# Performance work log

Hardware: AMD Instinct MI355X
Metric: run time of the kernel (lower is better)

Reference implementation:

```python
import jax, jax.numpy as jnp
import numpy as np

N = 50000   # nodes
E = 800000  # edges
D = 128     # in_dim == hidden_dim
L = 3       # 1 + hidden_layers(=2) SAGEConv layers
G = 64      # graphs in batch
C = 10      # classes


def setup_inputs() -> dict:
    key = jax.random.key(0)
    ks = jax.random.split(key, 10)
    h = jax.random.normal(ks[0], (N, D), dtype=jnp.float32)
    src = jax.random.randint(ks[1], (E,), 0, N, dtype=jnp.int32)
    dst = jax.random.randint(ks[2], (E,), 0, N, dtype=jnp.int32)
    graph_id = jnp.sort(jax.random.randint(ks[3], (N,), 0, G, dtype=jnp.int32))
    scale = 1.0 / np.sqrt(D)
    w_self = jax.random.normal(ks[4], (L, D, D), dtype=jnp.float32) * scale
    w_neigh = jax.random.normal(ks[5], (L, D, D), dtype=jnp.float32) * scale
    b = jax.random.normal(ks[6], (L, D), dtype=jnp.float32) * 0.01
    w_cls = jax.random.normal(ks[7], (D, C), dtype=jnp.float32) * scale
    b_cls = jax.random.normal(ks[8], (C,), dtype=jnp.float32) * 0.01
    return {"h": h, "src": src, "dst": dst, "graph_id": graph_id,
            "num_graphs": G, "w_self": w_self, "w_neigh": w_neigh,
            "b": b, "w_cls": w_cls, "b_cls": b_cls}


def reference(h, src, dst, graph_id, num_graphs, w_self, w_neigh, b, w_cls, b_cls):
    n = h.shape[0]
    # in-degree for mean aggregation (nodes with no in-edges -> 0 neigh feat)
    deg = jax.ops.segment_sum(jnp.ones((src.shape[0],), h.dtype), dst,
                              num_segments=n)
    inv_deg = (1.0 / jnp.maximum(deg, 1.0))[:, None]  # [N,1]
    for l in range(L):
        msg = h[src]                                           # gather [E,D]
        agg = jax.ops.segment_sum(msg, dst, num_segments=n) * inv_deg  # mean
        h = jax.nn.relu(h @ w_self[l] + agg @ w_neigh[l] + b[l])
    # mean_nodes readout over batched graphs
    counts = jax.ops.segment_sum(jnp.ones((n,), h.dtype), graph_id,
                                 num_segments=num_graphs)
    hg = jax.ops.segment_sum(h, graph_id, num_segments=num_graphs)
    hg = hg / jnp.maximum(counts, 1.0)[:, None]                # [G,D]
    return hg @ w_cls + b_cls                                  # [G,C]
```

## Files before the change

kernel.cpp:

```cpp
#include <hip/hip_runtime.h>

typedef short bf16x8 __attribute__((ext_vector_type(8)));
typedef float f32x4 __attribute__((ext_vector_type(4)));

#define DIM 128
#define NLAYER 3
#define NG 64
#define NC 10
#define NXCD 8
#define MAXDEG 64
#define LROWE 136

static __device__ __forceinline__ float b2f(unsigned short u) {
  union { unsigned int i; float f; } x; x.i = ((unsigned int)u) << 16; return x.f;
}
static __device__ __forceinline__ unsigned short f2b(float f) {
  unsigned int x = __float_as_uint(f);
  unsigned int r = (x + 0x7FFFu + ((x >> 16) & 1u)) >> 16;
  return (unsigned short)r;
}


__global__ __launch_bounds__(256) void k_prep(const float* __restrict__ h0,
    const float* __restrict__ wself, const float* __restrict__ wneigh,
    unsigned short* __restrict__ h_a, unsigned short* __restrict__ wtS,
    unsigned short* __restrict__ wtN, int* __restrict__ cur,
    float* __restrict__ hg, int n) {
  int tid = blockIdx.x * 256 + threadIdx.x;
  int nthr = gridDim.x * 256;
  for (int i = tid; i < n; i += nthr) cur[i] = 0;
  for (int i = tid; i < NG * DIM; i += nthr) hg[i] = 0.f;
  int tot4 = n * (DIM / 4);
  for (int i = tid; i < tot4; i += nthr) {
    float4 v = *(const float4*)(h0 + (size_t)i * 4);
    ushort4 r;
    r.x = f2b(v.x); r.y = f2b(v.y); r.z = f2b(v.z); r.w = f2b(v.w);
    *(ushort4*)(h_a + (size_t)i * 4) = r;
  }
  int totw = NLAYER * DIM * DIM;
  for (int i = tid; i < totw; i += nthr) {
    int l = i >> 14, rem = i & 16383, c = rem >> 7, k = rem & 127;
    int sidx = (l << 14) + (k << 7) + c;
    wtS[i] = f2b(wself[sidx]);
    wtN[i] = f2b(wneigh[sidx]);
  }
}


__global__ __launch_bounds__(256) void k_fillp(const int* __restrict__ src,
    const int* __restrict__ dst, int* __restrict__ cur, int* __restrict__ colxp,
    int e, int n) {
  int bucket = blockIdx.x & (NXCD - 1);
  int chunk = blockIdx.x >> 3, nchunk = gridDim.x >> 3;
  int bs = (n + NXCD - 1) / NXCD;
  int lo = bucket * bs, hi = min(n, lo + bs);
  for (int i = chunk * 256 + threadIdx.x; i < e; i += nchunk * 256) {
    int d = __builtin_nontemporal_load(dst + i);
    if (d >= lo && d < hi) {
      int p = atomicAdd(&cur[d], 1);
      if (p < MAXDEG) colxp[(size_t)d * MAXDEG + p] = __builtin_nontemporal_load(src + i);
    }
  }
}


__global__ __launch_bounds__(256, 4) void k_agg(const unsigned short* __restrict__ h,
    const int* __restrict__ cur, const int* __restrict__ colxp,
    unsigned short* __restrict__ agg, int n) {
  int wv = threadIdx.x >> 6, lane = threadIdx.x & 63;
  int v = blockIdx.x * 4 + wv;
  if (v >= n) return;
  int deg = cur[v];
  int end = min(deg, MAXDEG);
  const int4* cp4 = (const int4*)(colxp + (size_t)v * MAXDEG);
  int off = lane * 2;
  float a0[4], a1[4];
  #pragma unroll
  for (int k = 0; k < 4; ++k) { a0[k] = 0.f; a1[k] = 0.f; }
  for (int i = 0; i < end; i += 16) {
    int4 c0 = cp4[(i >> 2) + 0];
    int4 c1 = cp4[(i >> 2) + 1];
    int4 c2 = cp4[(i >> 2) + 2];
    int4 c3 = cp4[(i >> 2) + 3];
    int idxv[16] = {c0.x, c0.y, c0.z, c0.w, c1.x, c1.y, c1.z, c1.w,
                    c2.x, c2.y, c2.z, c2.w, c3.x, c3.y, c3.z, c3.w};
    unsigned int pk[16];
    #pragma unroll
    for (int k = 0; k < 16; ++k) {
      int s = (i + k < end) ? idxv[k] : 0;
      unsigned int p = *(const unsigned int*)(h + (size_t)s * DIM + off);
      pk[k] = (i + k < end) ? p : 0u;
    }
    #pragma unroll
    for (int k = 0; k < 16; ++k) {
      a0[k & 3] += __uint_as_float(pk[k] << 16);
      a1[k & 3] += __uint_as_float(pk[k] & 0xFFFF0000u);
    }
  }
  float s0 = (a0[0] + a0[1]) + (a0[2] + a0[3]);
  float s1 = (a1[0] + a1[1]) + (a1[2] + a1[3]);
  float w = 1.0f / fmaxf((float)deg, 1.0f);
  unsigned int outpk = (unsigned int)f2b(s0 * w) | ((unsigned int)f2b(s1 * w) << 16);
  *(unsigned int*)(agg + (size_t)v * DIM + off) = outpk;
}


__global__ __launch_bounds__(512, 2) void k_gemm(const unsigned short* __restrict__ hin,
    const unsigned short* __restrict__ agg, const unsigned short* __restrict__ wtS,
    const unsigned short* __restrict__ wtN, const float* __restrict__ bias,
    unsigned short* __restrict__ hout, int n) {
  __shared__ unsigned short ldsA[16 * LROWE];
  __shared__ unsigned short ldsG[16 * LROWE];
  int lane = threadIdx.x & 63, wv = threadIdx.x >> 6;
  int r = lane & 15, q = lane >> 4;
  int cf = wv;
  const unsigned short* wsp = wtS + (size_t)(cf * 16 + r) * DIM + q * 8;
  const unsigned short* wnp = wtN + (size_t)(cf * 16 + r) * DIM + q * 8;
  bf16x8 ws[4], wn[4];
  #pragma unroll
  for (int kf = 0; kf < 4; ++kf) {
    ws[kf] = *(const bf16x8*)(wsp + kf * 32);
    wn[kf] = *(const bf16x8*)(wnp + kf * 32);
  }
  int col = cf * 16 + r;
  float bval = bias[col];
  int ntiles = (n + 15) >> 4;
  int st = threadIdx.x & 255;
  int srow = st >> 4, schunk = st & 15;
  bool doG = threadIdx.x >= 256;
  for (int tb = blockIdx.x; tb < ntiles; tb += gridDim.x) {
    int row0 = tb * 16;
    {
      int grow = row0 + srow; if (grow > n - 1) grow = n - 1;
      const unsigned short* sp = (doG ? agg : hin) + (size_t)grow * DIM + schunk * 8;
      unsigned short* dp = (doG ? ldsG : ldsA) + srow * LROWE + schunk * 8;
      *(int4*)dp = *(const int4*)sp;
    }
    __syncthreads();
    bf16x8 ah[4], ag[4];
    #pragma unroll
    for (int kf = 0; kf < 4; ++kf) {
      ah[kf] = *(const bf16x8*)(ldsA + r * LROWE + q * 8 + kf * 32);
      ag[kf] = *(const bf16x8*)(ldsG + r * LROWE + q * 8 + kf * 32);
    }
    f32x4 acc = {0.f, 0.f, 0.f, 0.f};
    #pragma unroll
    for (int kf = 0; kf < 4; ++kf)
      acc = __builtin_amdgcn_mfma_f32_16x16x32_bf16(ah[kf], ws[kf], acc, 0, 0, 0);
    #pragma unroll
    for (int kf = 0; kf < 4; ++kf)
      acc = __builtin_amdgcn_mfma_f32_16x16x32_bf16(ag[kf], wn[kf], acc, 0, 0, 0);
    #pragma unroll
    for (int j = 0; j < 4; ++j) {
      int orow = row0 + q * 4 + j;
      if (orow < n) {
        float vv = acc[j] + bval;
        vv = vv > 0.f ? vv : 0.f;
        hout[(size_t)orow * DIM + col] = f2b(vv);
      }
    }
    __syncthreads();
  }
}


__global__ __launch_bounds__(256) void k_readout(const unsigned short* __restrict__ h,
    const int* __restrict__ gid, float* __restrict__ hg, int n) {
  int c = threadIdx.x & 127, half = threadIdx.x >> 7;
  int per = (n + gridDim.x - 1) / gridDim.x;
  int beg = blockIdx.x * per;
  int end = beg + per; if (end > n) end = n;
  int curg = -1;
  float acc = 0.f;
  for (int v = beg + half; v < end; v += 2) {
    int g = gid[v];
    if (g != curg) {
      if (curg >= 0) atomicAdd(&hg[curg * DIM + c], acc);
      curg = g; acc = 0.f;
    }
    acc += b2f(h[(size_t)v * DIM + c]);
  }
  if (curg >= 0) atomicAdd(&hg[curg * DIM + c], acc);
}


__global__ void k_head(const float* __restrict__ hg, const int* __restrict__ gid, int n,
    const float* __restrict__ wcls, const float* __restrict__ bcls,
    float* __restrict__ out) {
  __shared__ float sinv[NG];
  int t = threadIdx.x;
  if (t < NG) {
    int lo = 0, hi = n;
    while (lo < hi) { int mid = (lo + hi) >> 1; if (gid[mid] < t) lo = mid + 1; else hi = mid; }
    int lo2 = lo, hi2 = n;
    while (lo2 < hi2) { int mid = (lo2 + hi2) >> 1; if (gid[mid] < t + 1) lo2 = mid + 1; else hi2 = mid; }
    int cntg = lo2 - lo;
    sinv[t] = 1.0f / fmaxf((float)cntg, 1.0f);
  }
  __syncthreads();
  if (t >= NG * NC) return;
  int g = t / NC, c = t % NC;
  float s = 0.f;
  for (int k = 0; k < DIM; ++k) s += hg[g * DIM + k] * wcls[k * NC + c];
  out[t] = s * sinv[g] + bcls[c];
}


extern "C" void kernel_launch(void* const* d_in, const int* in_sizes, int n_in,
                              void* d_out, int out_size, void* d_ws, size_t ws_size,
                              hipStream_t stream) {
  const float* h0   = (const float*)d_in[0];
  const int* src    = (const int*)d_in[1];
  const int* dst    = (const int*)d_in[2];
  const int* gid    = (const int*)d_in[3];
  const float* wself  = (const float*)d_in[5];
  const float* wneigh = (const float*)d_in[6];
  const float* bias   = (const float*)d_in[7];
  const float* wcls   = (const float*)d_in[8];
  const float* bcls   = (const float*)d_in[9];
  int n = in_sizes[0] / DIM;
  int e = in_sizes[1];
  (void)n_in; (void)out_size; (void)ws_size;

  char* ws = (char*)d_ws;
  size_t o = 0;
  auto alloc = [&](size_t bytes) {
    char* p = ws + o;
    o = (o + bytes + 255) & ~(size_t)255;
    return p;
  };
  unsigned short* h_a   = (unsigned short*)alloc((size_t)n * DIM * 2);
  unsigned short* h_b   = (unsigned short*)alloc((size_t)n * DIM * 2);
  unsigned short* aggb  = (unsigned short*)alloc((size_t)n * DIM * 2);
  unsigned short* wtS   = (unsigned short*)alloc((size_t)NLAYER * DIM * DIM * 2);
  unsigned short* wtN   = (unsigned short*)alloc((size_t)NLAYER * DIM * DIM * 2);
  int*   cur   = (int*)alloc((size_t)n * 4);
  int*   colxp = (int*)alloc((size_t)n * MAXDEG * 4);
  float* hg    = (float*)alloc((size_t)NG * DIM * 4);

  k_prep<<<2048, 256, 0, stream>>>(h0, wself, wneigh, h_a, wtS, wtN, cur, hg, n);
  k_fillp<<<2048, 256, 0, stream>>>(src, dst, cur, colxp, e, n);

  const unsigned short* hin = h_a;
  unsigned short* hout = h_b;
  for (int l = 0; l < NLAYER; ++l) {
    k_agg<<<(n + 3) / 4, 256, 0, stream>>>(hin, cur, colxp, aggb, n);
    k_gemm<<<1024, 512, 0, stream>>>(hin, aggb, wtS + l * DIM * DIM,
                                     wtN + l * DIM * DIM, bias + l * DIM,
                                     hout, n);
    const unsigned short* t = hin;
    hin = hout;
    hout = (unsigned short*)t;
  }
  k_readout<<<512, 256, 0, stream>>>(hin, gid, hg, n);
  k_head<<<1, 640, 0, stream>>>(hg, gid, n, wcls, bcls, (float*)d_out);
}
```

Measured before the change: 222.8 us.

## Build padded adjacency via LDS-local counting, per-chunk scan, and LDS-cursor fill

Replaces the single fill kernel that used global atomics on a per-node cursor with a three-pass scheme. Each block counts in-edges for its node bucket and edge chunk in shared memory, a scan kernel turns the per-chunk counts into offsets and degrees, and a fill pass places source indices using shared-memory cursors. The aim is to remove contended global atomics and the cursor zeroing pass. In exchange the edge list is read twice, there are two extra launches, and a 32×N count array is written and read.

Result: slower. 335.4 us (+50.5%).

```diff
diff --git a/kernel.cpp b/kernel.cpp
--- a/kernel.cpp
+++ b/kernel.cpp
@@ -9,6 +9,7 @@
 #define NC 10
 #define NXCD 8
 #define MAXDEG 64
+#define NCHUNK 32
 #define LROWE 136
 
 static __device__ __forceinline__ float b2f(unsigned short u) {
@@ -24,11 +25,9 @@
 __global__ __launch_bounds__(256) void k_prep(const float* __restrict__ h0,
     const float* __restrict__ wself, const float* __restrict__ wneigh,
     unsigned short* __restrict__ h_a, unsigned short* __restrict__ wtS,
-    unsigned short* __restrict__ wtN, int* __restrict__ cur,
-    float* __restrict__ hg, int n) {
+    unsigned short* __restrict__ wtN, float* __restrict__ hg, int n) {
   int tid = blockIdx.x * 256 + threadIdx.x;
   int nthr = gridDim.x * 256;
-  for (int i = tid; i < n; i += nthr) cur[i] = 0;
   for (int i = tid; i < NG * DIM; i += nthr) hg[i] = 0.f;
   int tot4 = n * (DIM / 4);
   for (int i = tid; i < tot4; i += nthr) {
@@ -47,32 +46,76 @@
 }
 
 
-__global__ __launch_bounds__(256) void k_fillp(const int* __restrict__ src,
-    const int* __restrict__ dst, int* __restrict__ cur, int* __restrict__ colxp,
-    int e, int n) {
-  int bucket = blockIdx.x & (NXCD - 1);
-  int chunk = blockIdx.x >> 3, nchunk = gridDim.x >> 3;
+__global__ __launch_bounds__(256) void k_cnt(const int* __restrict__ dst,
+    int* __restrict__ cnt, int e, int n) {
+  int bucket = blockIdx.x & (NXCD - 1), chunk = blockIdx.x >> 3;
   int bs = (n + NXCD - 1) / NXCD;
   int lo = bucket * bs, hi = min(n, lo + bs);
-  for (int i = chunk * 256 + threadIdx.x; i < e; i += nchunk * 256) {
+  __shared__ int lcnt[6272];
+  for (int j = threadIdx.x; j < bs; j += 256) lcnt[j] = 0;
+  __syncthreads();
+  int ec = (e + NCHUNK - 1) / NCHUNK;
+  int ebeg = chunk * ec, eend = min(e, ebeg + ec);
+  for (int i = ebeg + threadIdx.x; i < eend; i += 256) {
+    int d = __builtin_nontemporal_load(dst + i);
+    if (d >= lo && d < hi) atomicAdd(&lcnt[d - lo], 1);
+  }
+  __syncthreads();
+  for (int j = threadIdx.x; j < bs; j += 256) {
+    int d = lo + j;
+    if (d < n) cnt[chunk * n + d] = lcnt[j];
+  }
+}
+
+
+__global__ __launch_bounds__(256) void k_scan(int* __restrict__ cnt,
+    int* __restrict__ deg, int n) {
+  int d = blockIdx.x * 256 + threadIdx.x;
+  if (d >= n) return;
+  int run = 0;
+  #pragma unroll
+  for (int c = 0; c < NCHUNK; ++c) {
+    int t = cnt[c * n + d];
+    cnt[c * n + d] = run;
+    run += t;
+  }
+  deg[d] = run;
+}
+
+
+__global__ __launch_bounds__(256) void k_fill(const int* __restrict__ src,
+    const int* __restrict__ dst, const int* __restrict__ cnt,
+    int* __restrict__ colxp, int e, int n) {
+  int bucket = blockIdx.x & (NXCD - 1), chunk = blockIdx.x >> 3;
+  int bs = (n + NXCD - 1) / NXCD;
+  int lo = bucket * bs, hi = min(n, lo + bs);
+  __shared__ int lcur[6272];
+  for (int j = threadIdx.x; j < bs; j += 256) {
+    int d = lo + j;
+    lcur[j] = (d < n) ? cnt[chunk * n + d] : 0;
+  }
+  __syncthreads();
+  int ec = (e + NCHUNK - 1) / NCHUNK;
+  int ebeg = chunk * ec, eend = min(e, ebeg + ec);
+  for (int i = ebeg + threadIdx.x; i < eend; i += 256) {
     int d = __builtin_nontemporal_load(dst + i);
     if (d >= lo && d < hi) {
-      int p = atomicAdd(&cur[d], 1);
-      if (p < MAXDEG) colxp[(size_t)d * MAXDEG + p] = __builtin_nontemporal_load(src + i);
+      int p = atomicAdd(&lcur[d - lo], 1);
+      if (p < MAXDEG) colxp[((size_t)d << 6) + p] = __builtin_nontemporal_load(src + i);
     }
   }
 }
 
 
 __global__ __launch_bounds__(256, 4) void k_agg(const unsigned short* __restrict__ h,
-    const int* __restrict__ cur, const int* __restrict__ colxp,
+    const int* __restrict__ deg_, const int* __restrict__ colxp,
     unsigned short* __restrict__ agg, int n) {
   int wv = threadIdx.x >> 6, lane = threadIdx.x & 63;
   int v = blockIdx.x * 4 + wv;
   if (v >= n) return;
-  int deg = cur[v];
+  int deg = deg_[v];
   int end = min(deg, MAXDEG);
-  const int4* cp4 = (const int4*)(colxp + (size_t)v * MAXDEG);
+  const int4* cp4 = (const int4*)(colxp + ((size_t)v << 6));
   int off = lane * 2;
   float a0[4], a1[4];
   #pragma unroll
@@ -234,17 +277,20 @@
   unsigned short* aggb  = (unsigned short*)alloc((size_t)n * DIM * 2);
   unsigned short* wtS   = (unsigned short*)alloc((size_t)NLAYER * DIM * DIM * 2);
   unsigned short* wtN   = (unsigned short*)alloc((size_t)NLAYER * DIM * DIM * 2);
-  int*   cur   = (int*)alloc((size_t)n * 4);
+  int*   deg   = (int*)alloc((size_t)n * 4);
+  int*   cnt   = (int*)alloc((size_t)NCHUNK * n * 4);
   int*   colxp = (int*)alloc((size_t)n * MAXDEG * 4);
   float* hg    = (float*)alloc((size_t)NG * DIM * 4);
 
-  k_prep<<<2048, 256, 0, stream>>>(h0, wself, wneigh, h_a, wtS, wtN, cur, hg, n);
-  k_fillp<<<2048, 256, 0, stream>>>(src, dst, cur, colxp, e, n);
+  k_prep<<<2048, 256, 0, stream>>>(h0, wself, wneigh, h_a, wtS, wtN, hg, n);
+  k_cnt<<<NXCD * NCHUNK, 256, 0, stream>>>(dst, cnt, e, n);
+  k_scan<<<(n + 255) / 256, 256, 0, stream>>>(cnt, deg, n);
+  k_fill<<<NXCD * NCHUNK, 256, 0, stream>>>(src, dst, cnt, colxp, e, n);
 
   const unsigned short* hin = h_a;
   unsigned short* hout = h_b;
   for (int l = 0; l < NLAYER; ++l) {
-    k_agg<<<(n + 3) / 4, 256, 0, stream>>>(hin, cur, colxp, aggb, n);
+    k_agg<<<(n + 3) / 4, 256, 0, stream>>>(hin, deg, colxp, aggb, n);
     k_gemm<<<1024, 512, 0, stream>>>(hin, aggb, wtS + l * DIM * DIM,
                                      wtN + l * DIM * DIM, bias + l * DIM,
                                      hout, n);
```
